# Kernel optimization log

Hardware: AMD Instinct MI355X
Metric: run time of the kernel (lower is better)

The kernel has to match this reference:

```python
import jax, jax.numpy as jnp
import numpy as np

B = 16
T_LEN, T_DIM = 149, 768
H = W = 56
S_DIM = 512
EPS = 1e-5


def setup_inputs() -> dict:
    key = jax.random.key(0)
    ks = jax.random.split(key, 12)
    N = H * W  # 3136
    return {
        "x": jax.random.normal(ks[0], (B, T_LEN, T_DIM), dtype=jnp.float32),
        "y": jax.random.normal(ks[1], (B, S_DIM, H, W), dtype=jnp.float32),
        # Conv1d(time_len -> h*w, k=1)
        "W_conv1": jax.random.normal(ks[2], (N, T_LEN), dtype=jnp.float32) * (1.0 / np.sqrt(T_LEN)),
        "b_conv1": jnp.zeros((N,), dtype=jnp.float32),
        # LayerNorms
        "ln1_g": jnp.ones((T_DIM,), dtype=jnp.float32),
        "ln1_b": jnp.zeros((T_DIM,), dtype=jnp.float32),
        "ln2_g": jnp.ones((S_DIM,), dtype=jnp.float32),
        "ln2_b": jnp.zeros((S_DIM,), dtype=jnp.float32),
        # positional encodings (1, C, H, W)
        "pe_wave": jax.random.normal(ks[3], (1, T_DIM, H, W), dtype=jnp.float32) * 0.02,
        "pe_spec": jax.random.normal(ks[4], (1, S_DIM, H, W), dtype=jnp.float32) * 0.02,
        # CrossAttention2D 1x1 convs
        "Wq": jax.random.normal(ks[5], (S_DIM, T_DIM), dtype=jnp.float32) * (1.0 / np.sqrt(T_DIM)),
        "bq": jnp.zeros((S_DIM,), dtype=jnp.float32),
        "Wk": jax.random.normal(ks[6], (S_DIM, S_DIM), dtype=jnp.float32) * (1.0 / np.sqrt(S_DIM)),
        "bk": jnp.zeros((S_DIM,), dtype=jnp.float32),
    }


def _layernorm(t, g, b):
    # t: (..., C), normalized over last axis
    m = jnp.mean(t, axis=-1, keepdims=True)
    v = jnp.mean(jnp.square(t - m), axis=-1, keepdims=True)
    return (t - m) * jax.lax.rsqrt(v + EPS) * g + b


def reference(x, y, W_conv1, b_conv1, ln1_g, ln1_b, ln2_g, ln2_b,
              pe_wave, pe_spec, Wq, bq, Wk, bk):
    # conv1d k=1 over channel dim time_len: (B,149,768) -> (B,3136,768)
    xe = jnp.einsum('bld,ol->bod', x, W_conv1) + b_conv1[None, :, None]
    # rearrange 'b (h w) c -> b h w c' (channel-last for LN/attention)
    nx = xe.reshape(x.shape[0], H, W, T_DIM)
    nx = _layernorm(nx, ln1_g, ln1_b) + pe_wave.transpose(0, 2, 3, 1)  # (B,H,W,768)

    ny = y.transpose(0, 2, 3, 1)  # (B,H,W,512)
    ny = _layernorm(ny, ln2_g, ln2_b) + pe_spec.transpose(0, 2, 3, 1)

    # 1x1 convs -> q, k; value is norm_y itself
    q = jnp.einsum('bhwc,oc->bhwo', nx, Wq) + bq  # (B,H,W,512)
    k = jnp.einsum('bhwc,oc->bhwo', ny, Wk) + bk  # (B,H,W,512)
    v = ny

    # row-local attention: each (b,h) row of W=56 tokens attends within itself
    scores = jnp.einsum('bhqc,bhkc->bhqk', q, k) / jnp.sqrt(jnp.float32(S_DIM))
    attn = jax.nn.softmax(scores, axis=-1)  # (B,H,W,W)
    out = jnp.einsum('bhqk,bhkc->bhqc', attn, v)  # (B,H,W,512)

    # permute back to (B,C,H,W), residual add
    return out.transpose(0, 3, 1, 2) + y
```

## Files before the change

### kernel.cpp

```cpp
#include <hip/hip_runtime.h>
#include <hip/hip_bf16.h>
#include <math.h>

typedef short bf16x8 __attribute__((ext_vector_type(8)));
typedef float f32x4 __attribute__((ext_vector_type(4)));

#define LN_EPS 1e-5f

static __device__ __forceinline__ float b2f(unsigned short u){
  unsigned int x = ((unsigned int)u) << 16; float f; __builtin_memcpy(&f,&x,4); return f;
}
static __device__ __forceinline__ unsigned short f2b(float f){
  unsigned int x; __builtin_memcpy(&x,&f,4);
  x += 0x7fffu + ((x>>16)&1u);
  return (unsigned short)(x>>16);
}

static __device__ __forceinline__ void gload_lds16(const void* g, void* l){
  __builtin_amdgcn_global_load_lds(
      (const __attribute__((address_space(1))) unsigned int*)g,
      (__attribute__((address_space(3))) unsigned int*)l, 16, 0, 0);
}

__global__ void pack_rowpad(const float* __restrict__ src, unsigned short* __restrict__ dst,
                            int rows, int srcK, int dstK, int rowsPad){
  int idx = blockIdx.x*256 + threadIdx.x;
  if (idx >= rowsPad*dstK) return;
  int r = idx / dstK, kk = idx - r*dstK;
  float v = (r < rows && kk < srcK) ? src[(size_t)r*srcK + kk] : 0.f;
  dst[idx] = f2b(v);
}

__global__ __launch_bounds__(256) void pack_xt(const float* __restrict__ x, unsigned short* __restrict__ xt){
  __shared__ float tile[32][33];
  int b = blockIdx.z;
  int l0 = blockIdx.y*32, d0 = blockIdx.x*32;
  int tl = threadIdx.x & 31, tw = threadIdx.x >> 5;
  for (int r=0;r<32;r+=8){
    int l = l0 + tw + r;
    tile[tw+r][tl] = (l<149) ? x[((size_t)b*149 + l)*768 + d0 + tl] : 0.f;
  }
  __syncthreads();
  for (int r=0;r<32;r+=8){
    int d = d0 + tw + r;
    int l = l0 + tl;
    if (l < 160) xt[((size_t)b*768 + d)*160 + l] = f2b(tile[tl][tw+r]);
  }
}

__global__ __launch_bounds__(256) void transpose_pe(const float* __restrict__ src, float* __restrict__ dst, int C){
  __shared__ float tile[32][33];
  int c0 = blockIdx.y*32, o0 = blockIdx.x*32;
  int tl = threadIdx.x & 31, tw = threadIdx.x >> 5;
  for (int r=0;r<32;r+=8)
    tile[tw+r][tl] = src[(size_t)(c0+tw+r)*3136 + o0 + tl];
  __syncthreads();
  for (int r=0;r<32;r+=8)
    dst[(size_t)(o0+tw+r)*C + c0 + tl] = tile[tl][tw+r];
}

#define GBM 128
#define GBN 128
#define GBK 32
__global__ __launch_bounds__(256)
void gemm_nt(const unsigned short* __restrict__ A, const unsigned short* __restrict__ Bt,
             unsigned short* __restrict__ C, const float* __restrict__ bias,
             int M, int N, int K, long long aStride, long long bStride, long long cStride,
             int swz8){
  __shared__ __align__(16) unsigned short As[GBM*GBK];
  __shared__ __align__(16) unsigned short Bs[GBN*GBK];
  int bx = blockIdx.x, by = blockIdx.y;
  if (swz8){
    int id = bx + gridDim.x*by;
    int xcd = id & 7, s = id >> 3;
    int q = s / gridDim.y;
    bx = xcd*(gridDim.x >> 3) + q;
    by = s - q*gridDim.y;
  }
  const unsigned short* Ab = A + (size_t)blockIdx.z*aStride;
  const unsigned short* Bb = Bt + (size_t)blockIdx.z*bStride;
  unsigned short* Cb = C + (size_t)blockIdx.z*cStride;
  int m0 = bx*GBM, n0 = by*GBN;
  int tid = threadIdx.x;
  int lane = tid & 63, wave = tid >> 6;
  int wm = (wave >> 1)*64, wn = (wave & 1)*64;
  f32x4 acc[4][4];
  #pragma unroll
  for (int i=0;i<4;i++)
    #pragma unroll
    for (int j=0;j<4;j++) acc[i][j]=(f32x4){0.f,0.f,0.f,0.f};
  int lr = lane & 15, lk = (lane >> 4)*8;
  for (int k0 = 0; k0 < K; k0 += GBK){
    #pragma unroll
    for (int p2=0;p2<2;p2++){
      int i = p2*256 + wave*64 + lane;
      gload_lds16(Ab + (size_t)(m0 + (i>>2))*K + k0 + (i&3)*8, As + (size_t)(p2*256 + wave*64)*8);
    }
    #pragma unroll
    for (int p2=0;p2<2;p2++){
      int i = p2*256 + wave*64 + lane;
      gload_lds16(Bb + (size_t)(n0 + (i>>2))*K + k0 + (i&3)*8, Bs + (size_t)(p2*256 + wave*64)*8);
    }
    __syncthreads();
    bf16x8 af[4], bfr[4];
    #pragma unroll
    for (int mi=0;mi<4;mi++) af[mi]  = *reinterpret_cast<const bf16x8*>(&As[(wm + mi*16 + lr)*GBK + lk]);
    #pragma unroll
    for (int nj=0;nj<4;nj++) bfr[nj] = *reinterpret_cast<const bf16x8*>(&Bs[(wn + nj*16 + lr)*GBK + lk]);
    #pragma unroll
    for (int mi=0;mi<4;mi++)
      #pragma unroll
      for (int nj=0;nj<4;nj++)
        acc[mi][nj] = __builtin_amdgcn_mfma_f32_16x16x32_bf16(af[mi], bfr[nj], acc[mi][nj], 0, 0, 0);
    __syncthreads();
  }
  int er = (lane >> 4)*4;
  #pragma unroll
  for (int mi=0;mi<4;mi++)
    #pragma unroll
    for (int nj=0;nj<4;nj++){
      int col = n0 + wn + nj*16 + lr;
      float bv = bias ? bias[col] : 0.f;
      #pragma unroll
      for (int e=0;e<4;e++){
        int row = m0 + wm + mi*16 + er + e;
        if (row < M) Cb[(size_t)row*N + col] = f2b(acc[mi][nj][e] + bv);
      }
    }
}

#define MFMA16(a,b,c) __builtin_amdgcn_mfma_f32_16x16x32_bf16(a,b,c,0,0,0)
__global__ __launch_bounds__(512)
void gemm256(const unsigned short* __restrict__ A, const unsigned short* __restrict__ Bt,
             unsigned short* __restrict__ C, const float* __restrict__ bias,
             int M, int N, int K){
  __shared__ __align__(16) unsigned short lds[65536];
  int tid = threadIdx.x;
  int lane = tid & 63, wave = tid >> 6;
  int wr = wave >> 2, wc = wave & 3;
  int lr = lane & 15, lo = lane >> 4;
  int cpx = gridDim.x >> 3;
  int id = blockIdx.x;
  int sid = (id & 7)*cpx + (id >> 3);
  int nby = N >> 8;
  int bx = sid / nby, by = sid - bx*nby;
  int m0 = bx << 8, n0 = by << 8;
  int NT = K >> 6;

  f32x4 acc[8][4];
  #pragma unroll
  for (int i=0;i<8;i++)
    #pragma unroll
    for (int j=0;j<4;j++) acc[i][j]=(f32x4){0.f,0.f,0.f,0.f};

  auto STAGE = [&](int t, int h){
    if (t >= NT) return;
    int buf = t & 1, tensor = h >> 1, half = h & 1;
    int k0 = t << 6;
    unsigned short* dstbase = lds + buf*32768 + tensor*16384;
    const unsigned short* srcT = tensor ? (Bt + (size_t)n0*K) : (A + (size_t)m0*K);
    #pragma unroll
    for (int ldi=0; ldi<2; ldi++){
      int c = half*1024 + ldi*512 + tid;
      int r = c >> 3;
      int l = (c & 7) ^ (r & 7);
      gload_lds16(srcT + (size_t)r*K + k0 + l*8,
                  dstbase + (half*1024 + ldi*512 + (wave<<6))*8);
    }
  };
  const char* ldsc = reinterpret_cast<const char*>(lds);
  int swz = lr & 7;
  auto rdA = [&](int buf, int mi, int kk)->bf16x8{
    int off = buf*65536 + (wr*128 + mi*16 + lr)*128 + (((kk*4+lo) ^ swz)*16);
    return *reinterpret_cast<const bf16x8*>(ldsc + off);
  };
  auto rdB = [&](int buf, int nj, int kk)->bf16x8{
    int off = buf*65536 + 32768 + (wc*64 + nj*16 + lr)*128 + (((kk*4+lo) ^ swz)*16);
    return *reinterpret_cast<const bf16x8*>(ldsc + off);
  };

  STAGE(0,0); STAGE(0,1); STAGE(0,2); STAGE(0,3); STAGE(1,0);
  asm volatile("s_waitcnt vmcnt(2)" ::: "memory");
  __builtin_amdgcn_s_barrier();

  for (int t=0; t<NT; ++t){
    int buf = t & 1;
    bf16x8 bf_[4][2], a0_[2][2], a1_[2][2];
    #pragma unroll
    for (int nj=0;nj<4;nj++){ bf_[nj][0]=rdB(buf,nj,0); bf_[nj][1]=rdB(buf,nj,1); }
    #pragma unroll
    for (int i=0;i<2;i++){ a0_[i][0]=rdA(buf,i,0);   a0_[i][1]=rdA(buf,i,1); }
    #pragma unroll
    for (int i=0;i<2;i++){ a1_[i][0]=rdA(buf,2+i,0); a1_[i][1]=rdA(buf,2+i,1); }
    STAGE(t+1, 1);
    __builtin_amdgcn_s_barrier();
    asm volatile("s_waitcnt lgkmcnt(0)" ::: "memory");
    __builtin_amdgcn_sched_barrier(0);
    __builtin_amdgcn_s_setprio(1);
    #pragma unroll
    for (int i=0;i<2;i++)
      #pragma unroll
      for (int nj=0;nj<4;nj++){
        acc[i][nj] = MFMA16(a0_[i][0], bf_[nj][0], acc[i][nj]);
        acc[i][nj] = MFMA16(a0_[i][1], bf_[nj][1], acc[i][nj]);
      }
    __builtin_amdgcn_s_setprio(0);
    __builtin_amdgcn_s_barrier();
    #pragma unroll
    for (int i=0;i<2;i++){ a0_[i][0]=rdA(buf,4+i,0); a0_[i][1]=rdA(buf,4+i,1); }
    STAGE(t+1, 2);
    __builtin_amdgcn_s_barrier();
    asm volatile("s_waitcnt lgkmcnt(0)" ::: "memory");
    __builtin_amdgcn_sched_barrier(0);
    __builtin_amdgcn_s_setprio(1);
    #pragma unroll
    for (int i=0;i<2;i++)
      #pragma unroll
      for (int nj=0;nj<4;nj++){
        acc[2+i][nj] = MFMA16(a1_[i][0], bf_[nj][0], acc[2+i][nj]);
        acc[2+i][nj] = MFMA16(a1_[i][1], bf_[nj][1], acc[2+i][nj]);
      }
    __builtin_amdgcn_s_setprio(0);
    __builtin_amdgcn_s_barrier();
    #pragma unroll
    for (int i=0;i<2;i++){ a1_[i][0]=rdA(buf,6+i,0); a1_[i][1]=rdA(buf,6+i,1); }
    STAGE(t+1, 3);
    __builtin_amdgcn_s_barrier();
    asm volatile("s_waitcnt lgkmcnt(0)" ::: "memory");
    __builtin_amdgcn_sched_barrier(0);
    __builtin_amdgcn_s_setprio(1);
    #pragma unroll
    for (int i=0;i<2;i++)
      #pragma unroll
      for (int nj=0;nj<4;nj++){
        acc[4+i][nj] = MFMA16(a0_[i][0], bf_[nj][0], acc[4+i][nj]);
        acc[4+i][nj] = MFMA16(a0_[i][1], bf_[nj][1], acc[4+i][nj]);
      }
    __builtin_amdgcn_s_setprio(0);
    __builtin_amdgcn_s_barrier();
    STAGE(t+2, 0);
    if (t < NT-2){
      asm volatile("s_waitcnt vmcnt(2)" ::: "memory");
    } else {
      asm volatile("s_waitcnt vmcnt(0)" ::: "memory");
    }
    __builtin_amdgcn_s_barrier();
    __builtin_amdgcn_s_setprio(1);
    #pragma unroll
    for (int i=0;i<2;i++)
      #pragma unroll
      for (int nj=0;nj<4;nj++){
        acc[6+i][nj] = MFMA16(a1_[i][0], bf_[nj][0], acc[6+i][nj]);
        acc[6+i][nj] = MFMA16(a1_[i][1], bf_[nj][1], acc[6+i][nj]);
      }
    __builtin_amdgcn_s_setprio(0);
    __builtin_amdgcn_s_barrier();
  }

  int er = lo*4;
  #pragma unroll
  for (int nj=0;nj<4;nj++){
    int col = n0 + wc*64 + nj*16 + lr;
    float bv = bias ? bias[col] : 0.f;
    #pragma unroll
    for (int mi=0;mi<8;mi++){
      int row = m0 + wr*128 + mi*16 + er;
      #pragma unroll
      for (int e=0;e<4;e++)
        C[(size_t)(row+e)*N + col] = f2b(acc[mi][nj][e] + bv);
    }
  }
}

__global__ __launch_bounds__(256) void ln1_kernel(unsigned short* __restrict__ xe,
    const float* __restrict__ g, const float* __restrict__ be, const float* __restrict__ pet){
  int b = blockIdx.y;
  int o0 = blockIdx.x*8;
  int t = threadIdx.x;
  int lane = t & 63, wv = t >> 6;
  __shared__ float ws1[4], ws2[4];
  __shared__ float mArr[8], rArr[8];
  float vals[8][3];
  #pragma unroll
  for (int oi=0;oi<8;oi++){
    size_t base = ((size_t)b*3136 + o0 + oi)*768;
    #pragma unroll
    for (int j=0;j<3;j++) vals[oi][j] = b2f(xe[base + t + 256*j]);
  }
  #pragma unroll
  for (int oi=0;oi<8;oi++){
    float s1=0.f, s2=0.f;
    #pragma unroll
    for (int j=0;j<3;j++){ float v=vals[oi][j]; s1+=v; s2+=v*v; }
    for (int d=32; d>0; d>>=1){ s1 += __shfl_xor(s1,d); s2 += __shfl_xor(s2,d); }
    if (lane==0){ ws1[wv]=s1; ws2[wv]=s2; }
    __syncthreads();
    if (t==0){
      float a=ws1[0]+ws1[1]+ws1[2]+ws1[3];
      float c=ws2[0]+ws2[1]+ws2[2]+ws2[3];
      float m=a*(1.f/768.f);
      float var=c*(1.f/768.f)-m*m;
      mArr[oi]=m; rArr[oi]=rsqrtf(var+LN_EPS);
    }
    __syncthreads();
  }
  #pragma unroll
  for (int oi=0;oi<8;oi++){
    size_t base = ((size_t)b*3136 + o0 + oi)*768;
    size_t pb = (size_t)(o0+oi)*768;
    float m=mArr[oi], r=rArr[oi];
    #pragma unroll
    for (int j=0;j<3;j++){
      int d = t + 256*j;
      xe[base+d] = f2b((vals[oi][j]-m)*r*g[d] + be[d] + pet[pb+d]);
    }
  }
}

__global__ __launch_bounds__(256) void ln2_kernel(const float* __restrict__ y,
    unsigned short* __restrict__ ny, unsigned short* __restrict__ nyT,
    const float* __restrict__ g, const float* __restrict__ bb, const float* __restrict__ pe){
  int b = blockIdx.y;
  int o0 = blockIdx.x*32;
  int t = threadIdx.x;
  int oi = t & 31, cg = t >> 5;
  __shared__ float red1[8][33], red2[8][33];
  __shared__ float mArr[32], rArr[32];
  __shared__ unsigned short tile[32][520];
  size_t ybase = (size_t)b*512*3136 + o0;
  float vals[64];
  float s1=0.f, s2=0.f;
  #pragma unroll
  for (int ci=0; ci<64; ci++){
    int c = cg*64 + ci;
    float v = y[ybase + (size_t)c*3136 + oi];
    vals[ci] = v;
    s1 += v; s2 += v*v;
  }
  red1[cg][oi]=s1; red2[cg][oi]=s2;
  __syncthreads();
  if (t < 32){
    float a=0.f, c2=0.f;
    #pragma unroll
    for (int kk=0;kk<8;kk++){ a+=red1[kk][t]; c2+=red2[kk][t]; }
    float m=a*(1.f/512.f);
    float var=c2*(1.f/512.f)-m*m;
    mArr[t]=m; rArr[t]=rsqrtf(var+LN_EPS);
  }
  __syncthreads();
  float m = mArr[oi], r = rArr[oi];
  #pragma unroll
  for (int ci=0; ci<64; ci++){
    int c = cg*64 + ci;
    float v = (vals[ci]-m)*r*g[c] + bb[c] + pe[(size_t)c*3136 + o0 + oi];
    tile[oi][c] = f2b(v);
  }
  __syncthreads();
  size_t nybase = ((size_t)b*3136 + o0)*512;
  for (int p = t; p < 32*64; p += 256){
    int oo = p >> 6, cp = (p & 63)*8;
    *reinterpret_cast<uint4*>(ny + nybase + (size_t)oo*512 + cp) =
        *reinterpret_cast<const uint4*>(&tile[oo][cp]);
  }
  for (int c2 = t; c2 < 512; c2 += 256){
    unsigned short row[32];
    #pragma unroll
    for (int o=0;o<32;o++) row[o] = tile[o][c2];
    size_t a = ((size_t)b*512 + c2)*3136 + o0;
    #pragma unroll
    for (int u=0;u<4;u++)
      *reinterpret_cast<uint4*>(nyT + a + u*8) = *reinterpret_cast<const uint4*>(&row[u*8]);
  }
}

__global__ __launch_bounds__(512) void attn_kernel(const unsigned short* __restrict__ q,
    const unsigned short* __restrict__ k, const unsigned short* __restrict__ vT,
    const float* __restrict__ y, float* __restrict__ outp){
  int h = blockIdx.x, b = blockIdx.y;
  int tid = threadIdx.x;
  int lane = tid & 63, w = tid >> 6;
  int wc = w & 3, wk = w >> 2;
  size_t base = (size_t)b*3136 + (size_t)h*56;
  __shared__ __align__(16) float SfP[2][56][60];
  __shared__ __align__(16) unsigned short Sb[64*64];

  f32x4 acc[4];
  #pragma unroll
  for (int mi=0;mi<4;mi++) acc[mi]=(f32x4){0.f,0.f,0.f,0.f};
  int lr = lane & 15, lo = lane >> 4;
  int lk = lo*8;
  int kr = wc*16 + lr; if (kr > 55) kr = 55;
  const unsigned short* krow = k + (base + kr)*512 + wk*256;
  const unsigned short* qrow = q + base*512 + wk*256;
  #pragma unroll
  for (int k0=0;k0<256;k0+=32){
    bf16x8 kf = *reinterpret_cast<const bf16x8*>(krow + k0 + lk);
    #pragma unroll
    for (int mi=0;mi<4;mi++){
      int qr = mi*16 + lr; if (qr > 55) qr = 55;
      bf16x8 qf = *reinterpret_cast<const bf16x8*>(qrow + (size_t)qr*512 + k0 + lk);
      acc[mi] = __builtin_amdgcn_mfma_f32_16x16x32_bf16(qf, kf, acc[mi], 0,0,0);
    }
  }

  const unsigned short* vb = vT + (size_t)b*512*3136 + (size_t)h*56;
  bf16x8 vfr[2][2][2];
  #pragma unroll
  for (int hp=0; hp<2; ++hp)
    #pragma unroll
    for (int kt=0;kt<2;++kt)
      #pragma unroll
      for (int mi=0;mi<2;++mi){
        int d = w*64 + hp*32 + mi*16 + lr;
        vfr[hp][kt][mi] = *reinterpret_cast<const bf16x8*>(vb + (size_t)d*3136 + kt*32 + lk);
      }

  int col = wc*16 + lr;
  int er = lo*4;
  if (col < 56){
    #pragma unroll
    for (int mi=0;mi<4;mi++)
      #pragma unroll
      for (int e=0;e<4;e++){
        int row = mi*16 + er + e;
        if (row < 56) SfP[wk][row][col] = acc[mi][e];
      }
  }
  __syncthreads();

  const float scale = 0.04419417382415922f;
  for (int r=0;r<7;r++){
    int i = w*7 + r;
    float xv = (lane<56) ? (SfP[0][i][lane] + SfP[1][i][lane])*scale : -1e30f;
    float mx = xv;
    #pragma unroll
    for (int d=32; d>0; d>>=1) mx = fmaxf(mx, __shfl_xor(mx,d));
    float ev = (lane<56) ? __expf(xv-mx) : 0.f;
    float sm = ev;
    #pragma unroll
    for (int d=32; d>0; d>>=1) sm += __shfl_xor(sm,d);
    unsigned short pv = (lane<56) ? f2b(ev/sm) : (unsigned short)0;
    int bo = i*128 + ((lane*2) ^ ((i&7)<<4));
    *reinterpret_cast<unsigned short*>(reinterpret_cast<char*>(Sb) + bo) = pv;
  }
  __syncthreads();

  bf16x8 pf[2][4];
  #pragma unroll
  for (int kt=0;kt<2;++kt)
    #pragma unroll
    for (int nj=0;nj<4;++nj){
      int row = nj*16 + lr;
      int bo = row*128 + (((kt*64) + lo*16) ^ ((row&7)<<4));
      pf[kt][nj] = *reinterpret_cast<const bf16x8*>(reinterpret_cast<const char*>(Sb) + bo);
    }

  #pragma unroll
  for (int hp=0; hp<2; ++hp){
    f32x4 a2[2][4];
    #pragma unroll
    for (int mi=0;mi<2;mi++)
      #pragma unroll
      for (int nj=0;nj<4;nj++) a2[mi][nj]=(f32x4){0.f,0.f,0.f,0.f};
    #pragma unroll
    for (int kt=0;kt<2;++kt)
      #pragma unroll
      for (int mi=0;mi<2;++mi)
        #pragma unroll
        for (int nj=0;nj<4;++nj)
          a2[mi][nj] = __builtin_amdgcn_mfma_f32_16x16x32_bf16(vfr[hp][kt][mi], pf[kt][nj], a2[mi][nj], 0,0,0);
    #pragma unroll
    for (int mi=0;mi<2;++mi)
      #pragma unroll
      for (int e=0;e<4;++e){
        size_t rowb = ((size_t)b*512 + w*64 + hp*32 + mi*16 + er + e)*3136 + (size_t)h*56;
        #pragma unroll
        for (int nj=0;nj<4;++nj){
          int r = nj*16 + lr;
          if (r < 56) outp[rowb + r] = a2[mi][nj][e] + y[rowb + r];
        }
      }
  }
}

extern "C" void kernel_launch(void* const* d_in, const int* in_sizes, int n_in,
                              void* d_out, int out_size, void* d_ws, size_t ws_size,
                              hipStream_t stream){
  const float* x   = (const float*)d_in[0];
  const float* y   = (const float*)d_in[1];
  const float* Wc  = (const float*)d_in[2];
  const float* g1  = (const float*)d_in[4];
  const float* be1 = (const float*)d_in[5];
  const float* g2  = (const float*)d_in[6];
  const float* be2 = (const float*)d_in[7];
  const float* peW = (const float*)d_in[8];
  const float* peS = (const float*)d_in[9];
  const float* Wq  = (const float*)d_in[10];
  const float* bq  = (const float*)d_in[11];
  const float* Wk  = (const float*)d_in[12];
  const float* bk  = (const float*)d_in[13];
  float* outp = (float*)d_out;

  char* p = (char*)d_ws;
  auto alloc = [&](size_t bytes)->char*{ char* r = p; p += (bytes + 255) & ~(size_t)255; return r; };
  unsigned short* WcB = (unsigned short*)alloc((size_t)3200*160*2);
  unsigned short* xt  = (unsigned short*)alloc((size_t)16*768*160*2);
  unsigned short* WqB = (unsigned short*)alloc((size_t)512*768*2);
  unsigned short* WkB = (unsigned short*)alloc((size_t)512*512*2);
  float* peWt = (float*)alloc((size_t)3136*768*4);
  unsigned short* xe  = (unsigned short*)alloc((size_t)16*3136*768*2);
  unsigned short* ny  = (unsigned short*)alloc((size_t)16*3136*512*2);
  unsigned short* nyT = (unsigned short*)alloc((size_t)16*512*3136*2 + 256);
  unsigned short* qb  = (unsigned short*)alloc((size_t)16*3136*512*2);
  unsigned short* kb  = (unsigned short*)alloc((size_t)16*3136*512*2);

  pack_rowpad<<<dim3((3200*160+255)/256), 256, 0, stream>>>(Wc, WcB, 3136, 149, 160, 3200);
  pack_rowpad<<<dim3((512*768+255)/256), 256, 0, stream>>>(Wq, WqB, 512, 768, 768, 512);
  pack_rowpad<<<dim3((512*512+255)/256), 256, 0, stream>>>(Wk, WkB, 512, 512, 512, 512);
  pack_xt<<<dim3(24,5,16), 256, 0, stream>>>(x, xt);
  transpose_pe<<<dim3(98,24), 256, 0, stream>>>(peW, peWt, 768);

  gemm_nt<<<dim3(25,6,16), 256, 0, stream>>>(WcB, xt, xe, nullptr, 3136, 768, 160,
                                             0LL, 768LL*160LL, 3136LL*768LL, 0);
  ln1_kernel<<<dim3(392,16), 256, 0, stream>>>(xe, g1, be1, peWt);
  ln2_kernel<<<dim3(98,16), 256, 0, stream>>>(y, ny, nyT, g2, be2, peS);
  gemm256<<<dim3(392), 512, 0, stream>>>(xe, WqB, qb, bq, 50176, 512, 768);
  gemm256<<<dim3(392), 512, 0, stream>>>(ny, WkB, kb, bk, 50176, 512, 512);
  attn_kernel<<<dim3(56,16), 512, 0, stream>>>(qb, kb, nyT, y, outp);
}
```

Measured before the change: 409.9 us.

## Merge Q/K projection GEMMs into one launch and split attention into two kernels

The Q and K projection GEMMs now run as a single 784-block launch, with each block picking its operand set from its swizzled block index. This is meant to fill the device better and remove one launch tail. Attention is split into a QK+softmax kernel that writes bf16 probabilities to a workspace buffer, and a separate PV kernel that spreads the 512 output channels over 4x more blocks to raise parallelism on the output-heavy stage. The cost is an extra global round trip for the probability matrix and one more launch.

```diff
diff --git a/kernel.cpp b/kernel.cpp
--- a/kernel.cpp
+++ b/kernel.cpp
@@ -131,9 +131,11 @@
 
 #define MFMA16(a,b,c) __builtin_amdgcn_mfma_f32_16x16x32_bf16(a,b,c,0,0,0)
 __global__ __launch_bounds__(512)
-void gemm256(const unsigned short* __restrict__ A, const unsigned short* __restrict__ Bt,
-             unsigned short* __restrict__ C, const float* __restrict__ bias,
-             int M, int N, int K){
+void gemm256_dual(const unsigned short* __restrict__ A0, const unsigned short* __restrict__ Bt0,
+                  unsigned short* __restrict__ C0, const float* __restrict__ bias0, int K0,
+                  const unsigned short* __restrict__ A1, const unsigned short* __restrict__ Bt1,
+                  unsigned short* __restrict__ C1, const float* __restrict__ bias1, int K1,
+                  int M, int N){
   __shared__ __align__(16) unsigned short lds[65536];
   int tid = threadIdx.x;
   int lane = tid & 63, wave = tid >> 6;
@@ -142,8 +144,14 @@
   int cpx = gridDim.x >> 3;
   int id = blockIdx.x;
   int sid = (id & 7)*cpx + (id >> 3);
+  int half = gridDim.x >> 1;
+  const unsigned short* A; const unsigned short* Bt; unsigned short* C;
+  const float* bias; int K;
+  int s2;
+  if (sid < half){ A=A0; Bt=Bt0; C=C0; bias=bias0; K=K0; s2=sid; }
+  else           { A=A1; Bt=Bt1; C=C1; bias=bias1; K=K1; s2=sid-half; }
   int nby = N >> 8;
-  int bx = sid / nby, by = sid - bx*nby;
+  int bx = s2 / nby, by = s2 - bx*nby;
   int m0 = bx << 8, n0 = by << 8;
   int NT = K >> 6;
 
@@ -155,17 +163,17 @@
 
   auto STAGE = [&](int t, int h){
     if (t >= NT) return;
-    int buf = t & 1, tensor = h >> 1, half = h & 1;
+    int buf = t & 1, tensor = h >> 1, hh = h & 1;
     int k0 = t << 6;
     unsigned short* dstbase = lds + buf*32768 + tensor*16384;
     const unsigned short* srcT = tensor ? (Bt + (size_t)n0*K) : (A + (size_t)m0*K);
     #pragma unroll
     for (int ldi=0; ldi<2; ldi++){
-      int c = half*1024 + ldi*512 + tid;
+      int c = hh*1024 + ldi*512 + tid;
       int r = c >> 3;
       int l = (c & 7) ^ (r & 7);
       gload_lds16(srcT + (size_t)r*K + k0 + l*8,
-                  dstbase + (half*1024 + ldi*512 + (wave<<6))*8);
+                  dstbase + (hh*1024 + ldi*512 + (wave<<6))*8);
     }
   };
   const char* ldsc = reinterpret_cast<const char*>(lds);
@@ -373,16 +381,14 @@
   }
 }
 
-__global__ __launch_bounds__(512) void attn_kernel(const unsigned short* __restrict__ q,
-    const unsigned short* __restrict__ k, const unsigned short* __restrict__ vT,
-    const float* __restrict__ y, float* __restrict__ outp){
+__global__ __launch_bounds__(512) void attn_qk(const unsigned short* __restrict__ q,
+    const unsigned short* __restrict__ k, unsigned short* __restrict__ Pb){
   int h = blockIdx.x, b = blockIdx.y;
   int tid = threadIdx.x;
   int lane = tid & 63, w = tid >> 6;
   int wc = w & 3, wk = w >> 2;
   size_t base = (size_t)b*3136 + (size_t)h*56;
   __shared__ __align__(16) float SfP[2][56][60];
-  __shared__ __align__(16) unsigned short Sb[64*64];
 
   f32x4 acc[4];
   #pragma unroll
@@ -403,18 +409,6 @@
     }
   }
 
-  const unsigned short* vb = vT + (size_t)b*512*3136 + (size_t)h*56;
-  bf16x8 vfr[2][2][2];
-  #pragma unroll
-  for (int hp=0; hp<2; ++hp)
-    #pragma unroll
-    for (int kt=0;kt<2;++kt)
-      #pragma unroll
-      for (int mi=0;mi<2;++mi){
-        int d = w*64 + hp*32 + mi*16 + lr;
-        vfr[hp][kt][mi] = *reinterpret_cast<const bf16x8*>(vb + (size_t)d*3136 + kt*32 + lk);
-      }
-
   int col = wc*16 + lr;
   int er = lo*4;
   if (col < 56){
@@ -428,6 +422,7 @@
   }
   __syncthreads();
 
+  unsigned short* Pbh = Pb + ((size_t)(b*56 + h))*4096;
   const float scale = 0.04419417382415922f;
   for (int r=0;r<7;r++){
     int i = w*7 + r;
@@ -440,47 +435,62 @@
     #pragma unroll
     for (int d=32; d>0; d>>=1) sm += __shfl_xor(sm,d);
     unsigned short pv = (lane<56) ? f2b(ev/sm) : (unsigned short)0;
-    int bo = i*128 + ((lane*2) ^ ((i&7)<<4));
-    *reinterpret_cast<unsigned short*>(reinterpret_cast<char*>(Sb) + bo) = pv;
-  }
-  __syncthreads();
-
-  bf16x8 pf[2][4];
+    Pbh[i*64 + lane] = pv;
+  }
+  Pbh[(56 + w)*64 + lane] = 0;
+}
+
+__global__ __launch_bounds__(256) void attn_pv(const unsigned short* __restrict__ vT,
+    const unsigned short* __restrict__ Pb, const float* __restrict__ y,
+    float* __restrict__ outp){
+  int dq = blockIdx.x, h = blockIdx.y, b = blockIdx.z;
+  int tid = threadIdx.x;
+  int lane = tid & 63, w = tid >> 6;
+  int lr = lane & 15, lo = lane >> 4;
+  int lk = lo*8;
+  int dbase = dq*128 + w*32;
+  const unsigned short* vb = vT + (size_t)b*512*3136 + (size_t)h*56;
+  const unsigned short* Pbh = Pb + ((size_t)(b*56 + h))*4096;
+
+  bf16x8 vfr[2][2], pf[2][4];
   #pragma unroll
   for (int kt=0;kt<2;++kt)
     #pragma unroll
-    for (int nj=0;nj<4;++nj){
-      int row = nj*16 + lr;
-      int bo = row*128 + (((kt*64) + lo*16) ^ ((row&7)<<4));
-      pf[kt][nj] = *reinterpret_cast<const bf16x8*>(reinterpret_cast<const char*>(Sb) + bo);
-    }
-
-  #pragma unroll
-  for (int hp=0; hp<2; ++hp){
-    f32x4 a2[2][4];
-    #pragma unroll
-    for (int mi=0;mi<2;mi++)
-      #pragma unroll
-      for (int nj=0;nj<4;nj++) a2[mi][nj]=(f32x4){0.f,0.f,0.f,0.f};
-    #pragma unroll
-    for (int kt=0;kt<2;++kt)
-      #pragma unroll
-      for (int mi=0;mi<2;++mi)
-        #pragma unroll
-        for (int nj=0;nj<4;++nj)
-          a2[mi][nj] = __builtin_amdgcn_mfma_f32_16x16x32_bf16(vfr[hp][kt][mi], pf[kt][nj], a2[mi][nj], 0,0,0);
+    for (int mi=0;mi<2;++mi){
+      int d = dbase + mi*16 + lr;
+      vfr[kt][mi] = *reinterpret_cast<const bf16x8*>(vb + (size_t)d*3136 + kt*32 + lk);
+    }
+  #pragma unroll
+  for (int kt=0;kt<2;++kt)
+    #pragma unroll
+    for (int nj=0;nj<4;++nj)
+      pf[kt][nj] = *reinterpret_cast<const bf16x8*>(Pbh + (nj*16 + lr)*64 + kt*32 + lk);
+
+  f32x4 a2[2][4];
+  #pragma unroll
+  for (int mi=0;mi<2;mi++)
+    #pragma unroll
+    for (int nj=0;nj<4;nj++) a2[mi][nj]=(f32x4){0.f,0.f,0.f,0.f};
+  #pragma unroll
+  for (int kt=0;kt<2;++kt)
     #pragma unroll
     for (int mi=0;mi<2;++mi)
       #pragma unroll
-      for (int e=0;e<4;++e){
-        size_t rowb = ((size_t)b*512 + w*64 + hp*32 + mi*16 + er + e)*3136 + (size_t)h*56;
-        #pragma unroll
-        for (int nj=0;nj<4;++nj){
-          int r = nj*16 + lr;
-          if (r < 56) outp[rowb + r] = a2[mi][nj][e] + y[rowb + r];
-        }
-      }
-  }
+      for (int nj=0;nj<4;++nj)
+        a2[mi][nj] = __builtin_amdgcn_mfma_f32_16x16x32_bf16(vfr[kt][mi], pf[kt][nj], a2[mi][nj], 0,0,0);
+
+  int er = lo*4;
+  #pragma unroll
+  for (int mi=0;mi<2;++mi)
+    #pragma unroll
+    for (int e=0;e<4;++e){
+      size_t rowb = ((size_t)b*512 + dbase + mi*16 + er + e)*3136 + (size_t)h*56;
+      #pragma unroll
+      for (int nj=0;nj<4;++nj){
+        int r = nj*16 + lr;
+        if (r < 56) outp[rowb + r] = a2[mi][nj][e] + y[rowb + r];
+      }
+    }
 }
 
 extern "C" void kernel_launch(void* const* d_in, const int* in_sizes, int n_in,
@@ -513,6 +523,7 @@
   unsigned short* nyT = (unsigned short*)alloc((size_t)16*512*3136*2 + 256);
   unsigned short* qb  = (unsigned short*)alloc((size_t)16*3136*512*2);
   unsigned short* kb  = (unsigned short*)alloc((size_t)16*3136*512*2);
+  unsigned short* Pb  = (unsigned short*)alloc((size_t)896*64*64*2);
 
   pack_rowpad<<<dim3((3200*160+255)/256), 256, 0, stream>>>(Wc, WcB, 3136, 149, 160, 3200);
   pack_rowpad<<<dim3((512*768+255)/256), 256, 0, stream>>>(Wq, WqB, 512, 768, 768, 512);
@@ -524,7 +535,8 @@
                                              0LL, 768LL*160LL, 3136LL*768LL, 0);
   ln1_kernel<<<dim3(392,16), 256, 0, stream>>>(xe, g1, be1, peWt);
   ln2_kernel<<<dim3(98,16), 256, 0, stream>>>(y, ny, nyT, g2, be2, peS);
-  gemm256<<<dim3(392), 512, 0, stream>>>(xe, WqB, qb, bq, 50176, 512, 768);
-  gemm256<<<dim3(392), 512, 0, stream>>>(ny, WkB, kb, bk, 50176, 512, 512);
-  attn_kernel<<<dim3(56,16), 512, 0, stream>>>(qb, kb, nyT, y, outp);
-}
+  gemm256_dual<<<dim3(784), 512, 0, stream>>>(xe, WqB, qb, bq, 768,
+                                              ny, WkB, kb, bk, 512, 50176, 512);
+  attn_qk<<<dim3(56,16), 512, 0, stream>>>(qb, kb, Pb);
+  attn_pv<<<dim3(4,56,16), 256, 0, stream>>>(nyT, Pb, y, outp);
+}
```

After: 429.6 us. 4.8% more time.
